# Kernel tuning notes

Measured on AMD Instinct MI355X. Metric: run time of the kernel, lower is better.

## Reference

```python
import jax, jax.numpy as jnp
import numpy as np

EPS = 1e-5
V = 65536      # number of surface vertices
E = 1048576    # number of neighbor points (~16 per vertex)
H = 128        # h_dim
CHEM_IN = 34   # 2 + num_gdf*2
GEOM_IN = 48   # num_gdf*2 + num_signatures


def _bn(x, p):
    # p: [4, dim] = (gamma, beta, running_mean, running_var); eval-mode BatchNorm1d
    g, b, m, v = p[0], p[1], p[2], p[3]
    return (x - m) * jax.lax.rsqrt(v + EPS) * g + b


def _mk_bn(key, dim):
    km, kv = jax.random.split(key)
    gamma = jnp.ones((dim,), jnp.float32)
    beta = jnp.zeros((dim,), jnp.float32)
    mean = 0.1 * jax.random.normal(km, (dim,), jnp.float32)
    var = 0.5 + jax.random.uniform(kv, (dim,), jnp.float32)  # strictly positive
    return jnp.stack([gamma, beta, mean, var])


def _mk_lin(key, din, dout):
    kw, kb = jax.random.split(key)
    s = 1.0 / np.sqrt(din)
    w = jax.random.uniform(kw, (din, dout), jnp.float32, -s, s)
    b = jax.random.uniform(kb, (dout,), jnp.float32, -s, s)
    return w, b


def setup_inputs() -> dict:
    key = jax.random.key(0)
    ks = jax.random.split(key, 16)
    chem_feats = jax.random.normal(ks[0], (E, CHEM_IN), jnp.float32)
    geom_feats = jax.random.normal(ks[1], (V, GEOM_IN), jnp.float32)
    nbr_vids = jax.random.randint(ks[2], (E,), 0, V, jnp.int64 if jax.config.jax_enable_x64 else jnp.int32)
    w1, b1 = _mk_lin(ks[3], CHEM_IN, H)
    w2, b2 = _mk_lin(ks[4], H, 2 * H)
    wg1, bg1 = _mk_lin(ks[5], GEOM_IN, H // 2)
    wg2, bg2 = _mk_lin(ks[6], H // 2, H // 2)
    wf1, bf1 = _mk_lin(ks[7], H + H // 2, H)
    wf2, bf2 = _mk_lin(ks[8], H, H)
    return {
        "chem_feats": chem_feats, "geom_feats": geom_feats, "nbr_vids": nbr_vids,
        "w1": w1, "b1": b1, "bn1": _mk_bn(ks[9], H),
        "w2": w2, "b2": b2, "bn2": _mk_bn(ks[10], 2 * H),
        "wg1": wg1, "bg1": bg1, "bng1": _mk_bn(ks[11], H // 2),
        "wg2": wg2, "bg2": bg2, "bng2": _mk_bn(ks[12], H // 2),
        "wf1": wf1, "bf1": bf1, "bnf1": _mk_bn(ks[13], H),
        "wf2": wf2, "bf2": bf2, "bnf2": _mk_bn(ks[14], H),
    }


def reference(chem_feats, geom_feats, nbr_vids,
              w1, b1, bn1, w2, b2, bn2,
              wg1, bg1, bng1, wg2, bg2, bng2,
              wf1, bf1, bnf1, wf2, bf2, bnf2):
    n_verts = geom_feats.shape[0]
    # chem_mlp: Linear -> (Dropout eval=id) -> BN -> SiLU -> Linear -> BN
    h = jax.nn.silu(_bn(chem_feats @ w1 + b1, bn1))
    h = _bn(h @ w2 + b2, bn2)                      # [E, 2H]
    nbr_filter, nbr_core = jnp.split(h, 2, axis=-1)
    h_chem = jax.nn.sigmoid(nbr_filter) * jax.nn.softplus(nbr_core)  # gated [E, H]
    h_chem = jax.ops.segment_sum(h_chem, nbr_vids, num_segments=n_verts)  # [V, H]
    # geom_mlp
    g = jax.nn.silu(_bn(geom_feats @ wg1 + bg1, bng1))
    h_geom = _bn(g @ wg2 + bg2, bng2)              # [V, H/2]
    # feat_mlp on concat
    x = jnp.concatenate([h_chem, h_geom], axis=-1)  # [V, 3H/2]
    x = jax.nn.silu(_bn(x @ wf1 + bf1, bnf1))
    h_out = _bn(x @ wf2 + bf2, bnf2)               # [V, H]
    return h_out
```

## Files before the change

kernel.cpp:

```cpp
#include <hip/hip_runtime.h>
#include <cstddef>

constexpr int V_CNT = 65536;
constexpr int E_CNT = 1048576;
constexpr int H_DIM = 128;
constexpr int CI = 34;
constexpr int GI = 48;
#define EPSF 1e-5f

typedef _Float16 f16;
typedef f16 f16x8 __attribute__((ext_vector_type(8)));
typedef float f32x4 __attribute__((ext_vector_type(4)));
#define MFMA16(a,b,c) __builtin_amdgcn_mfma_f32_16x16x32_f16(a,b,c,0,0,0)

__device__ __forceinline__ float sigmoidf_(float x){ return 1.0f/(1.0f+__expf(-x)); }
__device__ __forceinline__ float siluf_(float x){ return x/(1.0f+__expf(-x)); }
__device__ __forceinline__ float softplusf_(float x){
  return fmaxf(x,0.0f) + __logf(1.0f + __expf(-fabsf(x)));
}

__global__ __launch_bounds__(256) void prep_kernel(
    const float* __restrict__ w1, const float* __restrict__ b1, const float* __restrict__ bn1,
    const float* __restrict__ w2, const float* __restrict__ b2, const float* __restrict__ bn2,
    const float* __restrict__ wg1, const float* __restrict__ bg1, const float* __restrict__ bng1,
    const float* __restrict__ wg2, const float* __restrict__ bg2, const float* __restrict__ bng2,
    const float* __restrict__ wf1, const float* __restrict__ bf1, const float* __restrict__ bnf1,
    const float* __restrict__ wf2, const float* __restrict__ bf2, const float* __restrict__ bnf2,
    f16* __restrict__ w1f, float* __restrict__ shift1,
    f16* __restrict__ w2f, float* __restrict__ shift2,
    f16* __restrict__ wg1f, float* __restrict__ shiftg1,
    f16* __restrict__ wg2f, float* __restrict__ shiftg2,
    f16* __restrict__ wf1f, float* __restrict__ shiftf1,
    f16* __restrict__ wf2f, float* __restrict__ shiftf2)
{
  int t = blockIdx.x*256 + threadIdx.x;
  if (t < 128*64){
    int n = t>>6, k = t&63;
    float s = bn1[n]*rsqrtf(bn1[384+n]+EPSF);
    w1f[t] = (k<CI) ? (f16)(w1[k*128+n]*s) : (f16)0.f;
    if (k==0) shift1[n] = fmaf(s, b1[n]-bn1[256+n], bn1[128+n]);
  }
  if (t < 256*128){
    int n = t>>7, k = t&127;
    float s = bn2[n]*rsqrtf(bn2[768+n]+EPSF);
    w2f[t] = (f16)(w2[k*256+n]*s);
    if (k==0) shift2[n] = fmaf(s, b2[n]-bn2[512+n], bn2[256+n]);
  }
  if (t < 64*64){
    int n = t>>6, k = t&63;
    float s = bng1[n]*rsqrtf(bng1[192+n]+EPSF);
    wg1f[t] = (k<GI) ? (f16)(wg1[k*64+n]*s) : (f16)0.f;
    if (k==0) shiftg1[n] = fmaf(s, bg1[n]-bng1[128+n], bng1[64+n]);
  }
  if (t < 64*64){
    int n = t>>6, k = t&63;
    float s = bng2[n]*rsqrtf(bng2[192+n]+EPSF);
    wg2f[t] = (f16)(wg2[k*64+n]*s);
    if (k==0) shiftg2[n] = fmaf(s, bg2[n]-bng2[128+n], bng2[64+n]);
  }
  if (t < 128*192){
    int n = t/192, k = t - n*192;
    float s = bnf1[n]*rsqrtf(bnf1[384+n]+EPSF);
    wf1f[t] = (f16)(wf1[k*128+n]*s);
    if (k==0) shiftf1[n] = fmaf(s, bf1[n]-bnf1[256+n], bnf1[128+n]);
  }
  if (t < 128*128){
    int n = t>>7, k = t&127;
    float s = bnf2[n]*rsqrtf(bnf2[384+n]+EPSF);
    wf2f[t] = (f16)(wf2[k*128+n]*s);
    if (k==0) shiftf2[n] = fmaf(s, bf2[n]-bnf2[256+n], bnf2[128+n]);
  }
}

__global__ __launch_bounds__(256) void hist_kernel(const int* __restrict__ vids, int* __restrict__ counts){
  int i = blockIdx.x*blockDim.x + threadIdx.x;
  int stride = gridDim.x*blockDim.x;
  for(; i<E_CNT; i+=stride) atomicAdd(&counts[vids[i]], 1);
}

__global__ __launch_bounds__(1024) void scan_kernel(const int* __restrict__ counts,
                                                    int* __restrict__ offsets,
                                                    int* __restrict__ offsets_work){
  __shared__ int ps[1024];
  const int t = threadIdx.x;
  int4 c[16]; int s = 0;
  const int4* cp = (const int4*)counts + (size_t)t*16;
  #pragma unroll
  for(int i=0;i<16;i++){ c[i]=cp[i]; s += c[i].x+c[i].y+c[i].z+c[i].w; }
  ps[t]=s; __syncthreads();
  for(int d=1; d<1024; d<<=1){
    int v = (t>=d) ? ps[t-d] : 0;
    __syncthreads();
    ps[t] += v;
    __syncthreads();
  }
  int run = ps[t]-s;
  int4* o1 = (int4*)offsets + (size_t)t*16;
  int4* o2 = (int4*)offsets_work + (size_t)t*16;
  #pragma unroll
  for(int i=0;i<16;i++){
    int4 cc=c[i]; int4 o;
    o.x=run; run+=cc.x; o.y=run; run+=cc.y; o.z=run; run+=cc.z; o.w=run; run+=cc.w;
    o1[i]=o; o2[i]=o;
  }
  if(t==1023) offsets[65536] = run;
}

__global__ __launch_bounds__(256) void scatter_kernel(const int* __restrict__ vids,
                                                      int* __restrict__ offsets_work,
                                                      int* __restrict__ perm,
                                                      int* __restrict__ svid){
  int i = blockIdx.x*blockDim.x + threadIdx.x;
  int stride = gridDim.x*blockDim.x;
  for(; i<E_CNT; i+=stride){
    int v = vids[i];
    int pos = atomicAdd(&offsets_work[v], 1);
    perm[pos] = i;
    svid[pos] = v;
  }
}

__global__ __launch_bounds__(256) void geom_mfma(
    const float* __restrict__ geom,
    const f16* __restrict__ wg1f, const float* __restrict__ shg1,
    const f16* __restrict__ wg2f, const float* __restrict__ shg2,
    f16* __restrict__ dst, int stride, int colbase)
{
  __shared__ __align__(16) f16 Ag[64][72];
  const int t = threadIdx.x, w = t>>6, lane = t&63, n16 = lane&15, quad = lane>>4;
  const int v0 = blockIdx.x*64;
  const int col = w*16 + n16;

  for(int i=t;i<64*GI;i+=256){ int r=i/GI, k=i-r*GI; Ag[r][k] = (f16)geom[(size_t)v0*GI + i]; }
  { uint* Aw=(uint*)Ag; for(int i=t;i<64*8;i+=256){ int r=i>>3; Aw[r*36+24+(i&7)]=0u; } }

  f16x8 bg1[2], bg2[2];
  #pragma unroll
  for(int ks=0;ks<2;ks++){
    bg1[ks] = *(const f16x8*)(wg1f + (size_t)col*64 + ks*32 + quad*8);
    bg2[ks] = *(const f16x8*)(wg2f + (size_t)col*64 + ks*32 + quad*8);
  }
  __syncthreads();

  f32x4 c1[4];
  #pragma unroll
  for(int mt=0;mt<4;mt++) c1[mt] = (f32x4)(0.f);
  #pragma unroll
  for(int mt=0;mt<4;mt++)
    #pragma unroll
    for(int ks=0;ks<2;ks++){
      f16x8 a = *(const f16x8*)(&Ag[mt*16+n16][ks*32+quad*8]);
      c1[mt] = MFMA16(a, bg1[ks], c1[mt]);
    }
  __syncthreads();

  float s1 = shg1[col];
  #pragma unroll
  for(int mt=0;mt<4;mt++)
    #pragma unroll
    for(int r=0;r<4;r++)
      Ag[mt*16+quad*4+r][col] = (f16)siluf_(c1[mt][r] + s1);
  __syncthreads();

  f32x4 c2[4];
  #pragma unroll
  for(int mt=0;mt<4;mt++) c2[mt] = (f32x4)(0.f);
  #pragma unroll
  for(int mt=0;mt<4;mt++)
    #pragma unroll
    for(int ks=0;ks<2;ks++){
      f16x8 a = *(const f16x8*)(&Ag[mt*16+n16][ks*32+quad*8]);
      c2[mt] = MFMA16(a, bg2[ks], c2[mt]);
    }
  float s2 = shg2[col];
  #pragma unroll
  for(int mt=0;mt<4;mt++)
    #pragma unroll
    for(int r=0;r<4;r++)
      dst[(size_t)(v0 + mt*16+quad*4+r)*stride + colbase + col] = (f16)(c2[mt][r] + s2);
}

__global__ __launch_bounds__(256) void zero_f4(float4* p, int n4){
  int i = blockIdx.x*blockDim.x + threadIdx.x;
  int stride = gridDim.x*blockDim.x;
  float4 z; z.x=0.f; z.y=0.f; z.z=0.f; z.w=0.f;
  for(; i<n4; i+=stride) p[i] = z;
}

__global__ __launch_bounds__(256) void chem_fused(
    const float* __restrict__ chem,
    const int* __restrict__ perm, const int* __restrict__ svid,
    const f16* __restrict__ w1f, const float* __restrict__ shift1,
    const f16* __restrict__ w2f, const float* __restrict__ shift2,
    float* __restrict__ h_chem)
{
  __shared__ __align__(16) f16 A2[64][136];
  __shared__ __align__(16) f16 G[64][136];
  __shared__ int vid_s[64];
  const int t = threadIdx.x, w = t>>6, lane = t&63, n16 = lane&15, quad = lane>>4;
  const long p0 = (long)blockIdx.x*64;

  if(t<64) vid_s[t] = svid[p0+t];

  f16x8 b1[2][2];
  #pragma unroll
  for(int p=0;p<2;p++){
    int col = (2*w+p)*16 + n16;
    #pragma unroll
    for(int ks=0;ks<2;ks++)
      b1[p][ks] = *(const f16x8*)(w1f + (size_t)col*64 + ks*32 + quad*8);
  }
  float sh1v[2] = { shift1[(2*w+0)*16+n16], shift1[(2*w+1)*16+n16] };

  int pe[4];
  #pragma unroll
  for(int mt=0;mt<4;mt++) pe[mt] = perm[p0 + mt*16 + n16];

  f32x4 c1[4][2];
  #pragma unroll
  for(int mt=0;mt<4;mt++){ c1[mt][0]=(f32x4)(0.f); c1[mt][1]=(f32x4)(0.f); }
  #pragma unroll
  for(int mt=0;mt<4;mt++){
    const float* base = chem + (size_t)pe[mt]*CI;
    float2 u0 = *(const float2*)(base + quad*8 + 0);
    float2 u1 = *(const float2*)(base + quad*8 + 2);
    float2 u2 = *(const float2*)(base + quad*8 + 4);
    float2 u3 = *(const float2*)(base + quad*8 + 6);
    f16x8 a0;
    a0[0]=(f16)u0.x; a0[1]=(f16)u0.y; a0[2]=(f16)u1.x; a0[3]=(f16)u1.y;
    a0[4]=(f16)u2.x; a0[5]=(f16)u2.y; a0[6]=(f16)u3.x; a0[7]=(f16)u3.y;
    f16x8 a1 = (f16x8)(f16)0.f;
    if(quad==0){
      float2 uT = *(const float2*)(base + 32);
      a1[0]=(f16)uT.x; a1[1]=(f16)uT.y;
    }
    #pragma unroll
    for(int p=0;p<2;p++){
      c1[mt][p] = MFMA16(a0, b1[p][0], c1[mt][p]);
      c1[mt][p] = MFMA16(a1, b1[p][1], c1[mt][p]);
    }
  }
  #pragma unroll
  for(int mt=0;mt<4;mt++)
    #pragma unroll
    for(int p=0;p<2;p++){
      int col = (2*w+p)*16 + n16;
      #pragma unroll
      for(int r=0;r<4;r++)
        A2[mt*16+quad*4+r][col] = (f16)siluf_(c1[mt][p][r] + sh1v[p]);
    }
  __syncthreads();

  #pragma unroll 1
  for(int p=0;p<2;p++){
    const int gf = 2*w + p, gc = gf + 8;
    f16x8 b2f[4], b2c[4];
    #pragma unroll
    for(int ks=0;ks<4;ks++){
      b2f[ks] = *(const f16x8*)(w2f + (size_t)(gf*16+n16)*128 + ks*32 + quad*8);
      b2c[ks] = *(const f16x8*)(w2f + (size_t)(gc*16+n16)*128 + ks*32 + quad*8);
    }
    float shf = shift2[gf*16+n16];
    float shc = shift2[128 + gf*16+n16];
    f32x4 cf[4], cc_[4];
    #pragma unroll
    for(int mt=0;mt<4;mt++){ cf[mt]=(f32x4)(0.f); cc_[mt]=(f32x4)(0.f); }
    #pragma unroll
    for(int ks=0;ks<4;ks++){
      f16x8 a[4];
      #pragma unroll
      for(int mt=0;mt<4;mt++)
        a[mt] = *(const f16x8*)(&A2[mt*16+n16][ks*32+quad*8]);
      #pragma unroll
      for(int mt=0;mt<4;mt++){
        cf[mt]  = MFMA16(a[mt], b2f[ks], cf[mt]);
        cc_[mt] = MFMA16(a[mt], b2c[ks], cc_[mt]);
      }
    }
    #pragma unroll
    for(int mt=0;mt<4;mt++)
      #pragma unroll
      for(int r=0;r<4;r++){
        float f  = sigmoidf_(cf[mt][r]  + shf);
        float s  = softplusf_(cc_[mt][r] + shc);
        G[mt*16+quad*4+r][gf*16+n16] = (f16)(f*s);
      }
  }
  __syncthreads();

  {
    const int l = lane, g = w;
    const int e_beg = g*16, e_end = e_beg+16;
    float a0=0.f, a1=0.f;
    int cur = vid_s[e_beg];
    #pragma unroll 1
    for(int e=e_beg; e<e_end; ++e){
      int v = vid_s[e];
      if(v != cur){
        unsafeAtomicAdd(h_chem + (size_t)cur*H_DIM + 2*l,     a0);
        unsafeAtomicAdd(h_chem + (size_t)cur*H_DIM + 2*l + 1, a1);
        a0=0.f; a1=0.f; cur=v;
      }
      union{uint u; f16 h[2];} q;
      q.u = *(const uint*)&G[e][2*l];
      a0 += (float)q.h[0]; a1 += (float)q.h[1];
    }
    unsafeAtomicAdd(h_chem + (size_t)cur*H_DIM + 2*l,     a0);
    unsafeAtomicAdd(h_chem + (size_t)cur*H_DIM + 2*l + 1, a1);
  }
}

__global__ __launch_bounds__(256) void chem_atomic(
    const float* __restrict__ chem, const int* __restrict__ vids,
    const f16* __restrict__ w1f, const float* __restrict__ shift1,
    const f16* __restrict__ w2f, const float* __restrict__ shift2,
    float* __restrict__ h_chem)
{
  __shared__ __align__(16) f16 A2[64][136];
  __shared__ __align__(16) int vid_s[64];
  const int t = threadIdx.x, w = t>>6, lane = t&63, n16 = lane&15, quad = lane>>4;
  const long e0 = (long)blockIdx.x*64;

  if(t<64) vid_s[t] = vids[e0+t];

  f16x8 b1[2][2];
  #pragma unroll
  for(int p=0;p<2;p++){
    int col = (2*w+p)*16 + n16;
    #pragma unroll
    for(int ks=0;ks<2;ks++)
      b1[p][ks] = *(const f16x8*)(w1f + (size_t)col*64 + ks*32 + quad*8);
  }
  float sh1v[2] = { shift1[(2*w+0)*16+n16], shift1[(2*w+1)*16+n16] };

  f32x4 c1[4][2];
  #pragma unroll
  for(int mt=0;mt<4;mt++){ c1[mt][0]=(f32x4)(0.f); c1[mt][1]=(f32x4)(0.f); }
  #pragma unroll
  for(int mt=0;mt<4;mt++){
    const float* base = chem + (size_t)(e0 + mt*16 + n16)*CI;
    float2 u0 = *(const float2*)(base + quad*8 + 0);
    float2 u1 = *(const float2*)(base + quad*8 + 2);
    float2 u2 = *(const float2*)(base + quad*8 + 4);
    float2 u3 = *(const float2*)(base + quad*8 + 6);
    f16x8 a0;
    a0[0]=(f16)u0.x; a0[1]=(f16)u0.y; a0[2]=(f16)u1.x; a0[3]=(f16)u1.y;
    a0[4]=(f16)u2.x; a0[5]=(f16)u2.y; a0[6]=(f16)u3.x; a0[7]=(f16)u3.y;
    f16x8 a1 = (f16x8)(f16)0.f;
    if(quad==0){
      float2 uT = *(const float2*)(base + 32);
      a1[0]=(f16)uT.x; a1[1]=(f16)uT.y;
    }
    #pragma unroll
    for(int p=0;p<2;p++){
      c1[mt][p] = MFMA16(a0, b1[p][0], c1[mt][p]);
      c1[mt][p] = MFMA16(a1, b1[p][1], c1[mt][p]);
    }
  }
  #pragma unroll
  for(int mt=0;mt<4;mt++)
    #pragma unroll
    for(int p=0;p<2;p++){
      int col = (2*w+p)*16 + n16;
      #pragma unroll
      for(int r=0;r<4;r++)
        A2[mt*16+quad*4+r][col] = (f16)siluf_(c1[mt][p][r] + sh1v[p]);
    }
  const int ntab[4] = {2*w, 2*w+1, 2*w+8, 2*w+9};
  f16x8 b2[4][4];
  #pragma unroll
  for(int p=0;p<4;p++){
    int col = ntab[p]*16 + n16;
    #pragma unroll
    for(int ks=0;ks<4;ks++)
      b2[p][ks] = *(const f16x8*)(w2f + (size_t)col*128 + ks*32 + quad*8);
  }
  float shf[2] = { shift2[(2*w+0)*16+n16], shift2[(2*w+1)*16+n16] };
  float shc[2] = { shift2[128+(2*w+0)*16+n16], shift2[128+(2*w+1)*16+n16] };
  __syncthreads();

  f32x4 c2[4][4];
  #pragma unroll
  for(int mt=0;mt<4;mt++)
    #pragma unroll
    for(int p=0;p<4;p++) c2[mt][p] = (f32x4)(0.f);
  #pragma unroll
  for(int ks=0;ks<4;ks++){
    f16x8 a[4];
    #pragma unroll
    for(int mt=0;mt<4;mt++)
      a[mt] = *(const f16x8*)(&A2[mt*16+n16][ks*32+quad*8]);
    #pragma unroll
    for(int mt=0;mt<4;mt++)
      #pragma unroll
      for(int p=0;p<4;p++)
        c2[mt][p] = MFMA16(a[mt], b2[p][ks], c2[mt][p]);
  }
  #pragma unroll
  for(int mt=0;mt<4;mt++){
    int4 ev = *(const int4*)&vid_s[mt*16 + quad*4];
    int evv[4] = {ev.x, ev.y, ev.z, ev.w};
    #pragma unroll
    for(int p=0;p<2;p++){
      int colf = (2*w+p)*16 + n16;
      #pragma unroll
      for(int r=0;r<4;r++){
        float f  = sigmoidf_(c2[mt][p][r]   + shf[p]);
        float cc = softplusf_(c2[mt][p+2][r] + shc[p]);
        unsafeAtomicAdd(h_chem + (size_t)evv[r]*H_DIM + colf, f*cc);
      }
    }
  }
}

__global__ __launch_bounds__(256) void feat_split(
    const float* __restrict__ h_chem, const f16* __restrict__ h_geom,
    const f16* __restrict__ wf1f, const float* __restrict__ shf1,
    const f16* __restrict__ wf2f, const float* __restrict__ shf2,
    float* __restrict__ out)
{
  __shared__ __align__(16) f16 Af[64][200];
  const int t = threadIdx.x, w = t>>6, lane = t&63, n16 = lane&15, quad = lane>>4;
  const int v0 = blockIdx.x*64;

  for(int i=t;i<64*128;i+=256){ int r=i>>7, k=i&127; Af[r][k] = (f16)h_chem[(size_t)(v0+r)*128 + k]; }
  for(int i=t;i<64*64;i+=256){ int r=i>>6, k=i&63; Af[r][128+k] = h_geom[(size_t)(v0+r)*64 + k]; }

  f16x8 B1[2][6];
  #pragma unroll
  for(int p=0;p<2;p++){
    int col = (2*w+p)*16 + n16;
    #pragma unroll
    for(int ks=0;ks<6;ks++)
      B1[p][ks] = *(const f16x8*)(wf1f + (size_t)col*192 + ks*32 + quad*8);
  }
  __syncthreads();

  f32x4 c1[4][2];
  #pragma unroll
  for(int mt=0;mt<4;mt++){ c1[mt][0]=(f32x4)(0.f); c1[mt][1]=(f32x4)(0.f); }
  #pragma unroll
  for(int ks=0;ks<6;ks++){
    f16x8 a[4];
    #pragma unroll
    for(int mt=0;mt<4;mt++)
      a[mt] = *(const f16x8*)(&Af[mt*16+n16][ks*32+quad*8]);
    #pragma unroll
    for(int mt=0;mt<4;mt++)
      #pragma unroll
      for(int p=0;p<2;p++) c1[mt][p] = MFMA16(a[mt], B1[p][ks], c1[mt][p]);
  }
  __syncthreads();

  float s1v[2] = { shf1[(2*w+0)*16+n16], shf1[(2*w+1)*16+n16] };
  #pragma unroll
  for(int mt=0;mt<4;mt++)
    #pragma unroll
    for(int p=0;p<2;p++){
      int col = (2*w+p)*16 + n16;
      #pragma unroll
      for(int r=0;r<4;r++)
        Af[mt*16+quad*4+r][col] = (f16)siluf_(c1[mt][p][r] + s1v[p]);
    }
  __syncthreads();

  f16x8 B2[2][4];
  #pragma unroll
  for(int p=0;p<2;p++){
    int col = (2*w+p)*16 + n16;
    #pragma unroll
    for(int ks=0;ks<4;ks++)
      B2[p][ks] = *(const f16x8*)(wf2f + (size_t)col*128 + ks*32 + quad*8);
  }
  f32x4 c2[4][2];
  #pragma unroll
  for(int mt=0;mt<4;mt++){ c2[mt][0]=(f32x4)(0.f); c2[mt][1]=(f32x4)(0.f); }
  #pragma unroll
  for(int ks=0;ks<4;ks++){
    f16x8 a[4];
    #pragma unroll
    for(int mt=0;mt<4;mt++)
      a[mt] = *(const f16x8*)(&Af[mt*16+n16][ks*32+quad*8]);
    #pragma unroll
    for(int mt=0;mt<4;mt++)
      #pragma unroll
      for(int p=0;p<2;p++) c2[mt][p] = MFMA16(a[mt], B2[p][ks], c2[mt][p]);
  }
  float s2v[2] = { shf2[(2*w+0)*16+n16], shf2[(2*w+1)*16+n16] };
  #pragma unroll
  for(int mt=0;mt<4;mt++)
    #pragma unroll
    for(int p=0;p<2;p++){
      int col = (2*w+p)*16 + n16;
      #pragma unroll
      for(int r=0;r<4;r++)
        out[(size_t)(v0 + mt*16+quad*4+r)*128 + col] = c2[mt][p][r] + s2v[p];
    }
}

extern "C" void kernel_launch(void* const* d_in, const int* in_sizes, int n_in,
                              void* d_out, int out_size, void* d_ws, size_t ws_size,
                              hipStream_t stream) {
  const float* chem = (const float*)d_in[0];
  const float* geom = (const float*)d_in[1];
  const int*   vids = (const int*)d_in[2];
  const float* w1  = (const float*)d_in[3];
  const float* b1  = (const float*)d_in[4];
  const float* bn1 = (const float*)d_in[5];
  const float* w2  = (const float*)d_in[6];
  const float* b2  = (const float*)d_in[7];
  const float* bn2 = (const float*)d_in[8];
  const float* wg1 = (const float*)d_in[9];
  const float* bg1 = (const float*)d_in[10];
  const float* bng1= (const float*)d_in[11];
  const float* wg2 = (const float*)d_in[12];
  const float* bg2 = (const float*)d_in[13];
  const float* bng2= (const float*)d_in[14];
  const float* wf1 = (const float*)d_in[15];
  const float* bf1 = (const float*)d_in[16];
  const float* bnf1= (const float*)d_in[17];
  const float* wf2 = (const float*)d_in[18];
  const float* bf2 = (const float*)d_in[19];
  const float* bnf2= (const float*)d_in[20];
  float* out = (float*)d_out;
  char* ws = (char*)d_ws;

  const size_t NEED_BIG = 51301632ULL;
  const bool big = (ws_size >= NEED_BIG);

  if (big) {
    float* h_chem     = (float*)(ws + 0);
    f16*   h_geom     = (f16*)  (ws + 33554432);
    int*   perm       = (int*)  (ws + 41943040);
    int*   svid       = (int*)  (ws + 46137344);
    int*   counts     = (int*)  (ws + 50331648);
    int*   offsets    = (int*)  (ws + 50593792);
    int*   offsets_wk = (int*)  (ws + 50856192);
    char*  wb         = ws + 51118336;
    f16*   w1f  = (f16*)(wb);
    f16*   w2f  = (f16*)(wb + 16384);
    f16*   wg1f = (f16*)(wb + 81920);
    f16*   wg2f = (f16*)(wb + 90112);
    f16*   wf1f = (f16*)(wb + 98304);
    f16*   wf2f = (f16*)(wb + 147456);
    float* shift1  = (float*)(wb + 180224);
    float* shift2  = (float*)(wb + 180736);
    float* shiftg1 = (float*)(wb + 181760);
    float* shiftg2 = (float*)(wb + 182016);
    float* shiftf1 = (float*)(wb + 182272);
    float* shiftf2 = (float*)(wb + 182784);

    hipMemsetAsync(counts, 0, 65536*sizeof(int), stream);
    prep_kernel<<<dim3(128), dim3(256), 0, stream>>>(
        w1,b1,bn1, w2,b2,bn2, wg1,bg1,bng1, wg2,bg2,bng2, wf1,bf1,bnf1, wf2,bf2,bnf2,
        w1f,shift1, w2f,shift2, wg1f,shiftg1, wg2f,shiftg2, wf1f,shiftf1, wf2f,shiftf2);
    hist_kernel<<<dim3(1024), dim3(256), 0, stream>>>(vids, counts);
    scan_kernel<<<dim3(1), dim3(1024), 0, stream>>>(counts, offsets, offsets_wk);
    scatter_kernel<<<dim3(1024), dim3(256), 0, stream>>>(vids, offsets_wk, perm, svid);
    zero_f4<<<dim3(4096), dim3(256), 0, stream>>>((float4*)h_chem, V_CNT*H_DIM/4);
    geom_mfma<<<dim3(V_CNT/64), dim3(256), 0, stream>>>(geom, wg1f,shiftg1, wg2f,shiftg2, h_geom, 64, 0);
    chem_fused<<<dim3(E_CNT/64), dim3(256), 0, stream>>>(chem, perm, svid, w1f,shift1, w2f,shift2, h_chem);
    feat_split<<<dim3(V_CNT/64), dim3(256), 0, stream>>>(h_chem, h_geom, wf1f,shiftf1, wf2f,shiftf2, out);
  } else {
    float* h_chem = (float*)(ws + 0);
    f16*   h_geom = (f16*)  (ws + 33554432);
    char*  wb     = ws + 41943040;
    f16*   w1f  = (f16*)(wb);
    f16*   w2f  = (f16*)(wb + 16384);
    f16*   wg1f = (f16*)(wb + 81920);
    f16*   wg2f = (f16*)(wb + 90112);
    f16*   wf1f = (f16*)(wb + 98304);
    f16*   wf2f = (f16*)(wb + 147456);
    float* shift1  = (float*)(wb + 180224);
    float* shift2  = (float*)(wb + 180736);
    float* shiftg1 = (float*)(wb + 181760);
    float* shiftg2 = (float*)(wb + 182016);
    float* shiftf1 = (float*)(wb + 182272);
    float* shiftf2 = (float*)(wb + 182784);

    prep_kernel<<<dim3(128), dim3(256), 0, stream>>>(
        w1,b1,bn1, w2,b2,bn2, wg1,bg1,bng1, wg2,bg2,bng2, wf1,bf1,bnf1, wf2,bf2,bnf2,
        w1f,shift1, w2f,shift2, wg1f,shiftg1, wg2f,shiftg2, wf1f,shiftf1, wf2f,shiftf2);
    zero_f4<<<dim3(4096), dim3(256), 0, stream>>>((float4*)h_chem, V_CNT*H_DIM/4);
    geom_mfma<<<dim3(V_CNT/64), dim3(256), 0, stream>>>(geom, wg1f,shiftg1, wg2f,shiftg2, h_geom, 64, 0);
    chem_atomic<<<dim3(E_CNT/64), dim3(256), 0, stream>>>(chem, vids, w1f,shift1, w2f,shift2, h_chem);
    feat_split<<<dim3(V_CNT/64), dim3(256), 0, stream>>>(h_chem, h_geom, wf1f,shiftf1, wf2f,shiftf2, out);
  }
}
```

Measured before the change: 724.9 us.

## Fuse geom MLP into feature MLP, reuse LDS buffer, use fast reciprocal

Adds a feat_fused kernel that computes the geometry MLP in place of loading a precomputed h_geom, which removes the geom_mfma launch and the f16 h_geom round trip through global memory. In chem_fused, the gated layer-2 results are held in registers and written back into A2 instead of a separate G buffer, cutting LDS use to raise occupancy at the cost of one extra barrier. The zero_f4 kernel is replaced by hipMemsetAsync. Sigmoid and SiLU now use the hardware approximate reciprocal, which lowers precision slightly.

```diff
diff --git a/kernel.cpp b/kernel.cpp
--- a/kernel.cpp
+++ b/kernel.cpp
@@ -13,8 +13,9 @@
 typedef float f32x4 __attribute__((ext_vector_type(4)));
 #define MFMA16(a,b,c) __builtin_amdgcn_mfma_f32_16x16x32_f16(a,b,c,0,0,0)
 
-__device__ __forceinline__ float sigmoidf_(float x){ return 1.0f/(1.0f+__expf(-x)); }
-__device__ __forceinline__ float siluf_(float x){ return x/(1.0f+__expf(-x)); }
+__device__ __forceinline__ float frcp_(float x){ return __builtin_amdgcn_rcpf(x); }
+__device__ __forceinline__ float sigmoidf_(float x){ return frcp_(1.0f+__expf(-x)); }
+__device__ __forceinline__ float siluf_(float x){ return x*frcp_(1.0f+__expf(-x)); }
 __device__ __forceinline__ float softplusf_(float x){
   return fmaxf(x,0.0f) + __logf(1.0f + __expf(-fabsf(x)));
 }
@@ -180,13 +181,6 @@
       dst[(size_t)(v0 + mt*16+quad*4+r)*stride + colbase + col] = (f16)(c2[mt][r] + s2);
 }
 
-__global__ __launch_bounds__(256) void zero_f4(float4* p, int n4){
-  int i = blockIdx.x*blockDim.x + threadIdx.x;
-  int stride = gridDim.x*blockDim.x;
-  float4 z; z.x=0.f; z.y=0.f; z.z=0.f; z.w=0.f;
-  for(; i<n4; i+=stride) p[i] = z;
-}
-
 __global__ __launch_bounds__(256) void chem_fused(
     const float* __restrict__ chem,
     const int* __restrict__ perm, const int* __restrict__ svid,
@@ -195,7 +189,6 @@
     float* __restrict__ h_chem)
 {
   __shared__ __align__(16) f16 A2[64][136];
-  __shared__ __align__(16) f16 G[64][136];
   __shared__ int vid_s[64];
   const int t = threadIdx.x, w = t>>6, lane = t&63, n16 = lane&15, quad = lane>>4;
   const long p0 = (long)blockIdx.x*64;
@@ -251,8 +244,8 @@
     }
   __syncthreads();
 
-  #pragma unroll 1
-  for(int p=0;p<2;p++){
+  uint gp0[8], gp1[8];
+  auto l2pass = [&](const int p, uint* __restrict__ gp){
     const int gf = 2*w + p, gc = gf + 8;
     f16x8 b2f[4], b2c[4];
     #pragma unroll
@@ -280,12 +273,32 @@
     #pragma unroll
     for(int mt=0;mt<4;mt++)
       #pragma unroll
-      for(int r=0;r<4;r++){
-        float f  = sigmoidf_(cf[mt][r]  + shf);
-        float s  = softplusf_(cc_[mt][r] + shc);
-        G[mt*16+quad*4+r][gf*16+n16] = (f16)(f*s);
+      for(int j=0;j<2;j++){
+        float f0 = sigmoidf_(cf[mt][2*j]  +shf);
+        float s0 = softplusf_(cc_[mt][2*j]  +shc);
+        float f1 = sigmoidf_(cf[mt][2*j+1]+shf);
+        float s1 = softplusf_(cc_[mt][2*j+1]+shc);
+        union{uint u; f16 h[2];} q;
+        q.h[0]=(f16)(f0*s0); q.h[1]=(f16)(f1*s1);
+        gp[mt*2+j] = q.u;
       }
-  }
+  };
+  l2pass(0, gp0);
+  l2pass(1, gp1);
+  __syncthreads();
+
+  #pragma unroll
+  for(int mt=0;mt<4;mt++)
+    #pragma unroll
+    for(int j=0;j<2;j++){
+      union{uint u; f16 h[2];} q0, q1;
+      q0.u = gp0[mt*2+j]; q1.u = gp1[mt*2+j];
+      int row = mt*16+quad*4+2*j;
+      A2[row  ][(2*w+0)*16+n16] = q0.h[0];
+      A2[row+1][(2*w+0)*16+n16] = q0.h[1];
+      A2[row  ][(2*w+1)*16+n16] = q1.h[0];
+      A2[row+1][(2*w+1)*16+n16] = q1.h[1];
+    }
   __syncthreads();
 
   {
@@ -302,7 +315,7 @@
         a0=0.f; a1=0.f; cur=v;
       }
       union{uint u; f16 h[2];} q;
-      q.u = *(const uint*)&G[e][2*l];
+      q.u = *(const uint*)&A2[e][2*l];
       a0 += (float)q.h[0]; a1 += (float)q.h[1];
     }
     unsafeAtomicAdd(h_chem + (size_t)cur*H_DIM + 2*l,     a0);
@@ -411,6 +424,139 @@
       }
     }
   }
+}
+
+__global__ __launch_bounds__(256) void feat_fused(
+    const float* __restrict__ h_chem, const float* __restrict__ geom,
+    const f16* __restrict__ wg1f, const float* __restrict__ shg1,
+    const f16* __restrict__ wg2f, const float* __restrict__ shg2,
+    const f16* __restrict__ wf1f, const float* __restrict__ shf1,
+    const f16* __restrict__ wf2f, const float* __restrict__ shf2,
+    float* __restrict__ out)
+{
+  __shared__ __align__(16) f16 Af[64][200];
+  const int t = threadIdx.x, w = t>>6, lane = t&63, n16 = lane&15, quad = lane>>4;
+  const int v0 = blockIdx.x*64;
+
+  for(int i=t;i<64*128;i+=256){ int r=i>>7, k=i&127; Af[r][k] = (f16)h_chem[(size_t)(v0+r)*128 + k]; }
+  for(int i=t;i<64*GI;i+=256){ int r=i/GI, k=i-r*GI; Af[r][128+k] = (f16)geom[(size_t)v0*GI + i]; }
+  for(int i=t;i<64*16;i+=256){ int r=i>>4, k=i&15; Af[r][176+k] = (f16)0.f; }
+
+  const int gcol = w*16 + n16;
+  f16x8 bg1[2], bg2[2];
+  #pragma unroll
+  for(int ks=0;ks<2;ks++){
+    bg1[ks] = *(const f16x8*)(wg1f + (size_t)gcol*64 + ks*32 + quad*8);
+    bg2[ks] = *(const f16x8*)(wg2f + (size_t)gcol*64 + ks*32 + quad*8);
+  }
+  __syncthreads();
+
+  f32x4 cg[4];
+  #pragma unroll
+  for(int mt=0;mt<4;mt++) cg[mt]=(f32x4)(0.f);
+  #pragma unroll
+  for(int mt=0;mt<4;mt++)
+    #pragma unroll
+    for(int ks=0;ks<2;ks++){
+      f16x8 a = *(const f16x8*)(&Af[mt*16+n16][128 + ks*32+quad*8]);
+      cg[mt] = MFMA16(a, bg1[ks], cg[mt]);
+    }
+  __syncthreads();
+  float sg1 = shg1[gcol];
+  #pragma unroll
+  for(int mt=0;mt<4;mt++)
+    #pragma unroll
+    for(int r=0;r<4;r++)
+      Af[mt*16+quad*4+r][128+gcol] = (f16)siluf_(cg[mt][r] + sg1);
+  __syncthreads();
+  f32x4 cg2[4];
+  #pragma unroll
+  for(int mt=0;mt<4;mt++) cg2[mt]=(f32x4)(0.f);
+  #pragma unroll
+  for(int mt=0;mt<4;mt++)
+    #pragma unroll
+    for(int ks=0;ks<2;ks++){
+      f16x8 a = *(const f16x8*)(&Af[mt*16+n16][128 + ks*32+quad*8]);
+      cg2[mt] = MFMA16(a, bg2[ks], cg2[mt]);
+    }
+  __syncthreads();
+  float sg2 = shg2[gcol];
+  #pragma unroll
+  for(int mt=0;mt<4;mt++)
+    #pragma unroll
+    for(int r=0;r<4;r++)
+      Af[mt*16+quad*4+r][128+gcol] = (f16)(cg2[mt][r] + sg2);
+
+  f16x8 B1[2][6];
+  #pragma unroll
+  for(int p=0;p<2;p++){
+    int col = (2*w+p)*16 + n16;
+    #pragma unroll
+    for(int ks=0;ks<6;ks++)
+      B1[p][ks] = *(const f16x8*)(wf1f + (size_t)col*192 + ks*32 + quad*8);
+  }
+  __syncthreads();
+
+  f32x4 c1[4][2];
+  #pragma unroll
+  for(int mt=0;mt<4;mt++){ c1[mt][0]=(f32x4)(0.f); c1[mt][1]=(f32x4)(0.f); }
+  #pragma unroll
+  for(int ks=0;ks<6;ks++){
+    f16x8 a[4];
+    #pragma unroll
+    for(int mt=0;mt<4;mt++)
+      a[mt] = *(const f16x8*)(&Af[mt*16+n16][ks*32+quad*8]);
+    #pragma unroll
+    for(int mt=0;mt<4;mt++)
+      #pragma unroll
+      for(int p=0;p<2;p++) c1[mt][p] = MFMA16(a[mt], B1[p][ks], c1[mt][p]);
+  }
+  __syncthreads();
+
+  float s1v[2] = { shf1[(2*w+0)*16+n16], shf1[(2*w+1)*16+n16] };
+  #pragma unroll
+  for(int mt=0;mt<4;mt++)
+    #pragma unroll
+    for(int p=0;p<2;p++){
+      int col = (2*w+p)*16 + n16;
+      #pragma unroll
+      for(int r=0;r<4;r++)
+        Af[mt*16+quad*4+r][col] = (f16)siluf_(c1[mt][p][r] + s1v[p]);
+    }
+  __syncthreads();
+
+  f16x8 B2[2][4];
+  #pragma unroll
+  for(int p=0;p<2;p++){
+    int col = (2*w+p)*16 + n16;
+    #pragma unroll
+    for(int ks=0;ks<4;ks++)
+      B2[p][ks] = *(const f16x8*)(wf2f + (size_t)col*128 + ks*32 + quad*8);
+  }
+  f32x4 c2[4][2];
+  #pragma unroll
+  for(int mt=0;mt<4;mt++){ c2[mt][0]=(f32x4)(0.f); c2[mt][1]=(f32x4)(0.f); }
+  #pragma unroll
+  for(int ks=0;ks<4;ks++){
+    f16x8 a[4];
+    #pragma unroll
+    for(int mt=0;mt<4;mt++)
+      a[mt] = *(const f16x8*)(&Af[mt*16+n16][ks*32+quad*8]);
+    #pragma unroll
+    for(int mt=0;mt<4;mt++)
+      #pragma unroll
+      for(int p=0;p<2;p++) c2[mt][p] = MFMA16(a[mt], B2[p][ks], c2[mt][p]);
+  }
+  float s2v[2] = { shf2[(2*w+0)*16+n16], shf2[(2*w+1)*16+n16] };
+  #pragma unroll
+  for(int mt=0;mt<4;mt++)
+    #pragma unroll
+    for(int p=0;p<2;p++){
+      int col = (2*w+p)*16 + n16;
+      #pragma unroll
+      for(int r=0;r<4;r++)
+        out[(size_t)(v0 + mt*16+quad*4+r)*128 + col] = c2[mt][p][r] + s2v[p];
+    }
 }
 
 __global__ __launch_bounds__(256) void feat_split(
@@ -530,7 +676,6 @@
 
   if (big) {
     float* h_chem     = (float*)(ws + 0);
-    f16*   h_geom     = (f16*)  (ws + 33554432);
     int*   perm       = (int*)  (ws + 41943040);
     int*   svid       = (int*)  (ws + 46137344);
     int*   counts     = (int*)  (ws + 50331648);
@@ -551,16 +696,16 @@
     float* shiftf2 = (float*)(wb + 182784);
 
     hipMemsetAsync(counts, 0, 65536*sizeof(int), stream);
+    hipMemsetAsync(h_chem, 0, (size_t)V_CNT*H_DIM*sizeof(float), stream);
     prep_kernel<<<dim3(128), dim3(256), 0, stream>>>(
         w1,b1,bn1, w2,b2,bn2, wg1,bg1,bng1, wg2,bg2,bng2, wf1,bf1,bnf1, wf2,bf2,bnf2,
         w1f,shift1, w2f,shift2, wg1f,shiftg1, wg2f,shiftg2, wf1f,shiftf1, wf2f,shiftf2);
     hist_kernel<<<dim3(1024), dim3(256), 0, stream>>>(vids, counts);
     scan_kernel<<<dim3(1), dim3(1024), 0, stream>>>(counts, offsets, offsets_wk);
     scatter_kernel<<<dim3(1024), dim3(256), 0, stream>>>(vids, offsets_wk, perm, svid);
-    zero_f4<<<dim3(4096), dim3(256), 0, stream>>>((float4*)h_chem, V_CNT*H_DIM/4);
-    geom_mfma<<<dim3(V_CNT/64), dim3(256), 0, stream>>>(geom, wg1f,shiftg1, wg2f,shiftg2, h_geom, 64, 0);
     chem_fused<<<dim3(E_CNT/64), dim3(256), 0, stream>>>(chem, perm, svid, w1f,shift1, w2f,shift2, h_chem);
-    feat_split<<<dim3(V_CNT/64), dim3(256), 0, stream>>>(h_chem, h_geom, wf1f,shiftf1, wf2f,shiftf2, out);
+    feat_fused<<<dim3(V_CNT/64), dim3(256), 0, stream>>>(h_chem, geom,
+        wg1f,shiftg1, wg2f,shiftg2, wf1f,shiftf1, wf2f,shiftf2, out);
   } else {
     float* h_chem = (float*)(ws + 0);
     f16*   h_geom = (f16*)  (ws + 33554432);
@@ -578,10 +723,10 @@
     float* shiftf1 = (float*)(wb + 182272);
     float* shiftf2 = (float*)(wb + 182784);
 
+    hipMemsetAsync(h_chem, 0, (size_t)V_CNT*H_DIM*sizeof(float), stream);
     prep_kernel<<<dim3(128), dim3(256), 0, stream>>>(
         w1,b1,bn1, w2,b2,bn2, wg1,bg1,bng1, wg2,bg2,bng2, wf1,bf1,bnf1, wf2,bf2,bnf2,
         w1f,shift1, w2f,shift2, wg1f,shiftg1, wg2f,shiftg2, wf1f,shiftf1, wf2f,shiftf2);
-    zero_f4<<<dim3(4096), dim3(256), 0, stream>>>((float4*)h_chem, V_CNT*H_DIM/4);
     geom_mfma<<<dim3(V_CNT/64), dim3(256), 0, stream>>>(geom, wg1f,shiftg1, wg2f,shiftg2, h_geom, 64, 0);
     chem_atomic<<<dim3(E_CNT/64), dim3(256), 0, stream>>>(chem, vids, w1f,shift1, w2f,shift2, h_chem);
     feat_split<<<dim3(V_CNT/64), dim3(256), 0, stream>>>(h_chem, h_geom, wf1f,shiftf1, wf2f,shiftf2, out);
```

After: 675.7 us. 1.07x faster.
